# Kernel optimization log

Hardware: AMD Instinct MI355X
Metric: run time of the kernel (lower is better)

## Reference

```python
import jax, jax.numpy as jnp
import numpy as np

BS, C, H, W = 8, 128, 64, 64
CH = C // 2  # proj output channels


def setup_inputs() -> dict:
    key = jax.random.key(0)
    ks = jax.random.split(key, 8)
    s = 1.0 / np.sqrt(C)
    return {
        "tgt": jax.random.normal(ks[0], (BS, C, H, W), dtype=jnp.float32),
        "ref": jax.random.normal(ks[1], (BS, C, H, W), dtype=jnp.float32),
        "W_tgt": jax.random.normal(ks[2], (CH, C), dtype=jnp.float32) * s,
        "b_tgt": jax.random.normal(ks[3], (CH,), dtype=jnp.float32) * s,
        "W_ref": jax.random.normal(ks[4], (CH, C), dtype=jnp.float32) * s,
        "b_ref": jax.random.normal(ks[5], (CH,), dtype=jnp.float32) * s,
        "W_out": jax.random.normal(ks[6], (C, C), dtype=jnp.float32) * s,
        "b_out": jax.random.normal(ks[7], (C,), dtype=jnp.float32) * s,
    }


def reference(tgt, ref, W_tgt, b_tgt, W_ref, b_ref, W_out, b_out):
    bs, c, h, w = tgt.shape
    n = h * w
    # 1x1 conv == per-pixel matmul over channels; flatten spatial to tokens
    tgt_f = tgt.reshape(bs, c, n)              # [bs, c, n]
    ref_f = ref.reshape(bs, c, n)              # [bs, c, n]
    # att_tgt: [bs, n, c/2] ; att_ref: [bs, c/2, n] (ReLU after proj)
    att_tgt = jax.nn.relu(jnp.einsum('bcn,oc->bno', tgt_f, W_tgt) + b_tgt)
    att_ref = jax.nn.relu(jnp.einsum('bcn,oc->bon', ref_f, W_ref) + b_ref[None, :, None])
    pre_att = jnp.einsum('bnd,bdm->bnm', att_tgt, att_ref)   # [bs, n, n]
    att = jax.nn.softmax(pre_att, axis=-1)
    # fused tokens: [bs, n, c] = att @ ref_tokens
    fused = jnp.einsum('bnm,bcm->bnc', att, ref_f)
    fused = fused.transpose(0, 2, 1).reshape(bs, c, h, w)
    # output gate: 1x1 conv on tgt (no activation), elementwise mul
    att_out = jnp.einsum('bcn,oc->bon', tgt_f, W_out) + b_out[None, :, None]
    fused = fused * att_out.reshape(bs, c, h, w)
    return fused
```

## Files before the change

### kernel.cpp

```cpp
#include <hip/hip_runtime.h>

typedef __attribute__((ext_vector_type(8))) _Float16 f16x8;
typedef __attribute__((ext_vector_type(4))) float f32x4;

constexpr int kC  = 128;
constexpr int kCH = 64;
constexpr int kN  = 4096;
constexpr float kLog2e = 1.4426950408889634f;

__device__ __forceinline__ unsigned pkrtz(float a, float b) {
    union { __fp16 __attribute__((ext_vector_type(2))) v; unsigned u; } cv;
    cv.v = __builtin_amdgcn_cvt_pkrtz(a, b);
    return cv.u;
}

__device__ __forceinline__ float x2(float x) {
    return __builtin_amdgcn_exp2f(x);
}

__device__ __forceinline__ void g2l16(const unsigned short* g, unsigned short* l) {
    __builtin_amdgcn_global_load_lds(
        (const __attribute__((address_space(1))) unsigned int*)(g),
        (__attribute__((address_space(3))) unsigned int*)(l),
        16, 0, 0);
}

__global__ __launch_bounds__(256, 2) void proj_fused(
    const float* __restrict__ tgt, const float* __restrict__ ref,
    const float* __restrict__ Wt, const float* __restrict__ Wr,
    const float* __restrict__ Wo, const float* __restrict__ bt,
    const float* __restrict__ br, const float* __restrict__ bo,
    unsigned short* __restrict__ Qw, unsigned short* __restrict__ Kw,
    unsigned short* __restrict__ Vw, float* __restrict__ Gw)
{
    __shared__ __align__(16) unsigned short Xs[2][64 * 128];
    const int t = threadIdx.x;
    const int sl2 = blockIdx.y >> 3;
    const int b = blockIdx.y & 7;
    const int tok0 = blockIdx.x << 7;

    const int w = t >> 6, lane = t & 63;
    const int lg = (lane >> 4) & 3, lm = lane & 15;

    const float* X = sl2 ? ref : tgt;
    const float* Xb0 = X + ((size_t)b * kC) * kN + tok0;
    unsigned short* Vout = Vw + ((size_t)b * kC) * kN + tok0;

    const float* Wqk  = sl2 ? Wr : Wt;
    const float* bqk  = sl2 ? br : bt;
    const float scale = sl2 ? 1.0f : kLog2e;

    f16x8 wfq[4];
    float bq[4];
    {
        const int ocb = w * 16;
        #pragma unroll
        for (int ks = 0; ks < 4; ++ks) {
            const float* wp = Wqk + (size_t)(ocb + lm) * kC + ks * 32 + lg * 8;
            f32x4 f0 = *(const f32x4*)wp;
            f32x4 f1 = *(const f32x4*)(wp + 4);
            union { f16x8 h; uint4 u; } cv;
            cv.u = make_uint4(pkrtz(f0[0] * scale, f0[1] * scale),
                              pkrtz(f0[2] * scale, f0[3] * scale),
                              pkrtz(f1[0] * scale, f1[1] * scale),
                              pkrtz(f1[2] * scale, f1[3] * scale));
            wfq[ks] = cv.h;
        }
        #pragma unroll
        for (int r = 0; r < 4; ++r) bq[r] = bqk[ocb + lg * 4 + r] * scale;
    }

    f16x8 wfg[2][4];
    float bg[2][4];
    if (sl2 == 0) {
        const int ocb = w * 32;
        #pragma unroll
        for (int ot = 0; ot < 2; ++ot) {
            const int oc = ocb + ot * 16 + lm;
            #pragma unroll
            for (int ks = 0; ks < 4; ++ks) {
                const float* wp = Wo + (size_t)oc * kC + ks * 32 + lg * 8;
                f32x4 f0 = *(const f32x4*)wp;
                f32x4 f1 = *(const f32x4*)(wp + 4);
                union { f16x8 h; uint4 u; } cv;
                cv.u = make_uint4(pkrtz(f0[0], f0[1]), pkrtz(f0[2], f0[3]),
                                  pkrtz(f1[0], f1[1]), pkrtz(f1[2], f1[3]));
                wfg[ot][ks] = cv.h;
            }
            #pragma unroll
            for (int r = 0; r < 4; ++r) bg[ot][r] = bo[ocb + ot * 16 + lg * 4 + r];
        }
    }

    const int tk4 = (t & 15) * 4;
    const int c8  = (t >> 4) * 8;

    auto loadX = [&](int toff, f32x4* xv) {
        #pragma unroll
        for (int j = 0; j < 8; ++j)
            xv[j] = *(const f32x4*)(Xb0 + (size_t)(c8 + j) * kN + toff + tk4);
    };
    auto stageX = [&](const f32x4* xv, unsigned short* Xsb, int toff) {
        if (sl2 == 1) {
            #pragma unroll
            for (int j = 0; j < 8; ++j)
                *(uint2*)(Vout + (size_t)(c8 + j) * kN + toff + tk4) =
                    make_uint2(pkrtz(xv[j][0], xv[j][1]), pkrtz(xv[j][2], xv[j][3]));
        }
        #pragma unroll
        for (int s = 0; s < 4; ++s) {
            const int tok = tk4 + s;
            const int cc = (c8 >> 3) ^ (tok & 7);
            uint4 pk;
            pk.x = pkrtz(xv[0][s], xv[1][s]);
            pk.y = pkrtz(xv[2][s], xv[3][s]);
            pk.z = pkrtz(xv[4][s], xv[5][s]);
            pk.w = pkrtz(xv[6][s], xv[7][s]);
            *(uint4*)(Xsb + tok * 128 + cc * 8) = pk;
        }
    };
    auto compute = [&](const unsigned short* Xsb, int tokb) {
        unsigned short* outp = (sl2 ? Kw : Qw) + ((size_t)b * kN + tokb) * kCH;
        float* Gb = Gw + ((size_t)b * kC) * kN + tokb;
        const int ocq = w * 16;
        const int ocg = w * 32;
        #pragma unroll
        for (int ns = 0; ns < 4; ++ns) {
            const int tok = ns * 16 + lm;
            f16x8 xf[4];
            #pragma unroll
            for (int ks = 0; ks < 4; ++ks)
                xf[ks] = *(const f16x8*)(Xsb + tok * 128 +
                                         (((ks * 4 + lg) ^ (tok & 7)) << 3));
            {
                f32x4 acc = {bq[0], bq[1], bq[2], bq[3]};
                #pragma unroll
                for (int ks = 0; ks < 4; ++ks)
                    acc = __builtin_amdgcn_mfma_f32_16x16x32_f16(wfq[ks], xf[ks], acc, 0, 0, 0);
                uint2 pk;
                pk.x = pkrtz(fmaxf(acc[0], 0.f), fmaxf(acc[1], 0.f));
                pk.y = pkrtz(fmaxf(acc[2], 0.f), fmaxf(acc[3], 0.f));
                *(uint2*)(outp + (size_t)tok * kCH + ocq + lg * 4) = pk;
            }
            if (sl2 == 0) {
                #pragma unroll
                for (int ot = 0; ot < 2; ++ot) {
                    f32x4 acc = {bg[ot][0], bg[ot][1], bg[ot][2], bg[ot][3]};
                    #pragma unroll
                    for (int ks = 0; ks < 4; ++ks)
                        acc = __builtin_amdgcn_mfma_f32_16x16x32_f16(wfg[ot][ks], xf[ks], acc, 0, 0, 0);
                    #pragma unroll
                    for (int r = 0; r < 4; ++r)
                        Gb[(size_t)(ocg + ot * 16 + lg * 4 + r) * kN + tok] = acc[r];
                }
            }
        }
    };

    f32x4 xv[8], xw[8];
    loadX(0, xv);
    stageX(xv, Xs[0], 0);
    __syncthreads();
    loadX(64, xw);
    compute(Xs[0], tok0);
    stageX(xw, Xs[1], 64);
    __syncthreads();
    compute(Xs[1], tok0 + 64);
}

__global__ __launch_bounds__(256, 2) void flash7_kernel(
    const unsigned short* __restrict__ Qw,
    const unsigned short* __restrict__ Kw,
    const unsigned short* __restrict__ Vw,
    const float* __restrict__ Gw,
    float* __restrict__ out)
{
    __shared__ __align__(16) unsigned short Ks[2][64 * 64];
    __shared__ __align__(16) unsigned short Vs[2][128 * 64];
    __shared__ __align__(16) unsigned short Ps[64 * 64];

    const int t = threadIdx.x;
    const int b = blockIdx.x & 7;
    const int n0 = (blockIdx.x >> 3) << 6;
    const int w = t >> 6, lane = t & 63;
    const int lg = (lane >> 4) & 3, lm = lane & 15;
    const int row_q = w * 16 + lm;
    const int swz = lm & 7;

    const unsigned short* Qb = Qw + ((size_t)b * kN) * kCH;
    const unsigned short* Kb = Kw + ((size_t)b * kN) * kCH;
    const unsigned short* Vb = Vw + ((size_t)b * kC) * kN;

    f16x8 qf0 = *(const f16x8*)(Qb + (size_t)(n0 + row_q) * kCH + (lg << 3));
    f16x8 qf1 = *(const f16x8*)(Qb + (size_t)(n0 + row_q) * kCH + 32 + (lg << 3));

    const int srow = t >> 3, scol = t & 7;
    const int sco  = (scol ^ (srow & 7)) << 3;
    const int wv   = t >> 6;

    const int fswz0 = (lg ^ swz) << 3;
    const int fswz1 = ((4 | lg) ^ swz) << 3;
    int psw[4];
    #pragma unroll
    for (int mb = 0; mb < 4; ++mb)
        psw[mb] = row_q * 64 + (((2 * mb + (lg >> 1)) ^ swz) << 3) + ((lg & 1) << 2);

    union { f16x8 h; uint4 u; } onec;
    onec.u = make_uint4(0x3c003c00u, 0x3c003c00u, 0x3c003c00u, 0x3c003c00u);
    const f16x8 onev = onec.h;

    f32x4 O[8];
    #pragma unroll
    for (int cb = 0; cb < 8; ++cb) O[cb] = (f32x4){0.f, 0.f, 0.f, 0.f};
    f32x4 L = (f32x4){0.f, 0.f, 0.f, 0.f};
    float m_run = 0.0f;

    unsigned short* Ks0 = Ks[0]; unsigned short* Ks1 = Ks[1];
    unsigned short* Vs0 = Vs[0]; unsigned short* Vs1 = Vs[1];

    auto stage = [&](unsigned short* Kd, unsigned short* Vd, int m0) {
        g2l16(Kb + (size_t)(m0 + srow) * kCH + sco,      Kd + wv * 512);
        g2l16(Kb + (size_t)(m0 + 32 + srow) * kCH + sco, Kd + 2048 + wv * 512);
        #pragma unroll
        for (int j = 0; j < 4; ++j)
            g2l16(Vb + (size_t)(32 * j + srow) * kN + m0 + sco,
                  Vd + j * 2048 + wv * 512);
    };
    stage(Ks0, Vs0, 0);

    auto tile = [&](const unsigned short* Kc, const unsigned short* Vc,
                    unsigned short* Kn, unsigned short* Vn, int kt) {
        __syncthreads();
        if (kt + 1 < kN / 64) stage(Kn, Vn, (kt + 1) << 6);

        f32x4 s[4];
        __builtin_amdgcn_s_setprio(1);
        #pragma unroll
        for (int mb = 0; mb < 4; ++mb) {
            const unsigned short* kr = Kc + ((mb * 16 + lm) << 6);
            f16x8 kf0 = *(const f16x8*)(kr + fswz0);
            f16x8 kf1 = *(const f16x8*)(kr + fswz1);
            f32x4 acc = (f32x4){0.f, 0.f, 0.f, 0.f};
            acc = __builtin_amdgcn_mfma_f32_16x16x32_f16(kf0, qf0, acc, 0, 0, 0);
            acc = __builtin_amdgcn_mfma_f32_16x16x32_f16(kf1, qf1, acc, 0, 0, 0);
            s[mb] = acc;
        }
        __builtin_amdgcn_s_setprio(0);

        float mloc = 0.0f;
        #pragma unroll
        for (int mb = 0; mb < 4; ++mb)
            #pragma unroll
            for (int r = 0; r < 4; ++r) mloc = fmaxf(mloc, s[mb][r]);
        mloc = fmaxf(mloc, __shfl_xor(mloc, 16, 64));
        mloc = fmaxf(mloc, __shfl_xor(mloc, 32, 64));
        const bool upd = __any(mloc > m_run);
        const float mnew = upd ? fmaxf(m_run, mloc) : m_run;

        #pragma unroll
        for (int mb = 0; mb < 4; ++mb) {
            unsigned plo = pkrtz(x2(s[mb][0] - mnew), x2(s[mb][1] - mnew));
            unsigned phi = pkrtz(x2(s[mb][2] - mnew), x2(s[mb][3] - mnew));
            *(uint2*)(Ps + psw[mb]) = make_uint2(plo, phi);
        }

        if (upd) {
            float alpha = x2(m_run - mnew);
            float a0 = __shfl(alpha, (lg << 2) + 0, 64);
            float a1 = __shfl(alpha, (lg << 2) + 1, 64);
            float a2 = __shfl(alpha, (lg << 2) + 2, 64);
            float a3 = __shfl(alpha, (lg << 2) + 3, 64);
            #pragma unroll
            for (int cb = 0; cb < 8; ++cb) {
                O[cb][0] *= a0; O[cb][1] *= a1; O[cb][2] *= a2; O[cb][3] *= a3;
            }
            L[0] *= a0; L[1] *= a1; L[2] *= a2; L[3] *= a3;
            m_run = mnew;
        }

        f16x8 pf0 = *(const f16x8*)(Ps + row_q * 64 + fswz0);
        f16x8 pf1 = *(const f16x8*)(Ps + row_q * 64 + fswz1);
        __builtin_amdgcn_s_setprio(1);
        L = __builtin_amdgcn_mfma_f32_16x16x32_f16(pf0, onev, L, 0, 0, 0);
        L = __builtin_amdgcn_mfma_f32_16x16x32_f16(pf1, onev, L, 0, 0, 0);
        #pragma unroll
        for (int cb = 0; cb < 8; ++cb) {
            const unsigned short* vr = Vc + ((cb * 16 + lm) << 6);
            f16x8 vf0 = *(const f16x8*)(vr + fswz0);
            f16x8 vf1 = *(const f16x8*)(vr + fswz1);
            O[cb] = __builtin_amdgcn_mfma_f32_16x16x32_f16(pf0, vf0, O[cb], 0, 0, 0);
            O[cb] = __builtin_amdgcn_mfma_f32_16x16x32_f16(pf1, vf1, O[cb], 0, 0, 0);
        }
        __builtin_amdgcn_s_setprio(0);
    };

    for (int kt = 0; kt < kN / 64; kt += 2) {
        tile(Ks0, Vs0, Ks1, Vs1, kt);
        tile(Ks1, Vs1, Ks0, Vs0, kt + 1);
    }

    const float i0 = 1.0f / L[0], i1 = 1.0f / L[1];
    const float i2 = 1.0f / L[2], i3 = 1.0f / L[3];
    const float* Gb = Gw + ((size_t)b * kC) * kN;
    float* Ob = out + ((size_t)b * kC) * kN;
    #pragma unroll
    for (int cb = 0; cb < 8; ++cb) {
        int c = cb * 16 + lm;
        size_t base = (size_t)c * kN + n0 + w * 16 + (lg << 2);
        float4 g = *(const float4*)(Gb + base);
        float4 res;
        res.x = O[cb][0] * i0 * g.x;
        res.y = O[cb][1] * i1 * g.y;
        res.z = O[cb][2] * i2 * g.z;
        res.w = O[cb][3] * i3 * g.w;
        *(float4*)(Ob + base) = res;
    }
}

extern "C" void kernel_launch(void* const* d_in, const int* in_sizes, int n_in,
                              void* d_out, int out_size, void* d_ws, size_t ws_size,
                              hipStream_t stream) {
    const float* tgt   = (const float*)d_in[0];
    const float* ref   = (const float*)d_in[1];
    const float* W_tgt = (const float*)d_in[2];
    const float* b_tgt = (const float*)d_in[3];
    const float* W_ref = (const float*)d_in[4];
    const float* b_ref = (const float*)d_in[5];
    const float* W_out = (const float*)d_in[6];
    const float* b_out = (const float*)d_in[7];
    float* out = (float*)d_out;

    const size_t QK = (size_t)8 * kN * kCH;
    const size_t CV = (size_t)8 * kC * kN;
    unsigned short* Qw = (unsigned short*)d_ws;
    unsigned short* Kw = Qw + QK;
    unsigned short* Vw = Kw + QK;
    float*          Gw = (float*)(Vw + CV);

    proj_fused<<<dim3(32, 16), 256, 0, stream>>>(tgt, ref, W_tgt, W_ref, W_out,
                                                 b_tgt, b_ref, b_out, Qw, Kw, Vw, Gw);
    flash7_kernel<<<dim3(512), 256, 0, stream>>>(Qw, Kw, Vw, Gw, out);
}
```

Measured before the change: 183.4 us.

## Process two query sub-tiles per wave to double K/V reuse per block

Each wave now handles 32 query rows (two 16-row halves), so a block covers 128 queries instead of 64 and every K/V tile staged in shared memory feeds twice as many MFMAs. This halves global and LDS traffic for K and V per query. The cost is a doubled O accumulator set and more registers per thread, so launch bounds drop to one block per SM. The grid shrinks to 256 blocks, which may leave some of the 256 CUs underused or lower latency hiding.

```diff
diff --git a/kernel.cpp b/kernel.cpp
--- a/kernel.cpp
+++ b/kernel.cpp
@@ -168,7 +168,7 @@
     compute(Xs[1], tok0 + 64);
 }
 
-__global__ __launch_bounds__(256, 2) void flash7_kernel(
+__global__ __launch_bounds__(256, 1) void flash8_kernel(
     const unsigned short* __restrict__ Qw,
     const unsigned short* __restrict__ Kw,
     const unsigned short* __restrict__ Vw,
@@ -177,22 +177,27 @@
 {
     __shared__ __align__(16) unsigned short Ks[2][64 * 64];
     __shared__ __align__(16) unsigned short Vs[2][128 * 64];
-    __shared__ __align__(16) unsigned short Ps[64 * 64];
+    __shared__ __align__(16) unsigned short Ps[128 * 64];
 
     const int t = threadIdx.x;
     const int b = blockIdx.x & 7;
-    const int n0 = (blockIdx.x >> 3) << 6;
+    const int n0 = (blockIdx.x >> 3) << 7;
     const int w = t >> 6, lane = t & 63;
     const int lg = (lane >> 4) & 3, lm = lane & 15;
-    const int row_q = w * 16 + lm;
+    const int qw0 = w * 32;
     const int swz = lm & 7;
 
     const unsigned short* Qb = Qw + ((size_t)b * kN) * kCH;
     const unsigned short* Kb = Kw + ((size_t)b * kN) * kCH;
     const unsigned short* Vb = Vw + ((size_t)b * kC) * kN;
 
-    f16x8 qf0 = *(const f16x8*)(Qb + (size_t)(n0 + row_q) * kCH + (lg << 3));
-    f16x8 qf1 = *(const f16x8*)(Qb + (size_t)(n0 + row_q) * kCH + 32 + (lg << 3));
+    f16x8 qf[2][2];
+    #pragma unroll
+    for (int h = 0; h < 2; ++h) {
+        const unsigned short* qp = Qb + (size_t)(n0 + qw0 + h * 16 + lm) * kCH;
+        qf[h][0] = *(const f16x8*)(qp + (lg << 3));
+        qf[h][1] = *(const f16x8*)(qp + 32 + (lg << 3));
+    }
 
     const int srow = t >> 3, scol = t & 7;
     const int sco  = (scol ^ (srow & 7)) << 3;
@@ -200,20 +205,25 @@
 
     const int fswz0 = (lg ^ swz) << 3;
     const int fswz1 = ((4 | lg) ^ swz) << 3;
-    int psw[4];
+    int psw[2][4];
     #pragma unroll
-    for (int mb = 0; mb < 4; ++mb)
-        psw[mb] = row_q * 64 + (((2 * mb + (lg >> 1)) ^ swz) << 3) + ((lg & 1) << 2);
+    for (int h = 0; h < 2; ++h)
+        #pragma unroll
+        for (int mb = 0; mb < 4; ++mb)
+            psw[h][mb] = (qw0 + h * 16 + lm) * 64 +
+                         (((2 * mb + (lg >> 1)) ^ swz) << 3) + ((lg & 1) << 2);
 
     union { f16x8 h; uint4 u; } onec;
     onec.u = make_uint4(0x3c003c00u, 0x3c003c00u, 0x3c003c00u, 0x3c003c00u);
     const f16x8 onev = onec.h;
 
-    f32x4 O[8];
+    f32x4 O[2][8];
     #pragma unroll
-    for (int cb = 0; cb < 8; ++cb) O[cb] = (f32x4){0.f, 0.f, 0.f, 0.f};
-    f32x4 L = (f32x4){0.f, 0.f, 0.f, 0.f};
-    float m_run = 0.0f;
+    for (int h = 0; h < 2; ++h)
+        #pragma unroll
+        for (int cb = 0; cb < 8; ++cb) O[h][cb] = (f32x4){0.f, 0.f, 0.f, 0.f};
+    f32x4 L[2] = {(f32x4){0.f, 0.f, 0.f, 0.f}, (f32x4){0.f, 0.f, 0.f, 0.f}};
+    float m_run[2] = {0.0f, 0.0f};
 
     unsigned short* Ks0 = Ks[0]; unsigned short* Ks1 = Ks[1];
     unsigned short* Vs0 = Vs[0]; unsigned short* Vs1 = Vs[1];
@@ -233,63 +243,91 @@
         __syncthreads();
         if (kt + 1 < kN / 64) stage(Kn, Vn, (kt + 1) << 6);
 
-        f32x4 s[4];
+        f32x4 s[2][4];
         __builtin_amdgcn_s_setprio(1);
         #pragma unroll
         for (int mb = 0; mb < 4; ++mb) {
             const unsigned short* kr = Kc + ((mb * 16 + lm) << 6);
             f16x8 kf0 = *(const f16x8*)(kr + fswz0);
             f16x8 kf1 = *(const f16x8*)(kr + fswz1);
-            f32x4 acc = (f32x4){0.f, 0.f, 0.f, 0.f};
-            acc = __builtin_amdgcn_mfma_f32_16x16x32_f16(kf0, qf0, acc, 0, 0, 0);
-            acc = __builtin_amdgcn_mfma_f32_16x16x32_f16(kf1, qf1, acc, 0, 0, 0);
-            s[mb] = acc;
+            #pragma unroll
+            for (int h = 0; h < 2; ++h) {
+                f32x4 acc = (f32x4){0.f, 0.f, 0.f, 0.f};
+                acc = __builtin_amdgcn_mfma_f32_16x16x32_f16(kf0, qf[h][0], acc, 0, 0, 0);
+                acc = __builtin_amdgcn_mfma_f32_16x16x32_f16(kf1, qf[h][1], acc, 0, 0, 0);
+                s[h][mb] = acc;
+            }
         }
         __builtin_amdgcn_s_setprio(0);
 
-        float mloc = 0.0f;
-        #pragma unroll
-        for (int mb = 0; mb < 4; ++mb)
-            #pragma unroll
-            for (int r = 0; r < 4; ++r) mloc = fmaxf(mloc, s[mb][r]);
-        mloc = fmaxf(mloc, __shfl_xor(mloc, 16, 64));
-        mloc = fmaxf(mloc, __shfl_xor(mloc, 32, 64));
-        const bool upd = __any(mloc > m_run);
-        const float mnew = upd ? fmaxf(m_run, mloc) : m_run;
-
-        #pragma unroll
-        for (int mb = 0; mb < 4; ++mb) {
-            unsigned plo = pkrtz(x2(s[mb][0] - mnew), x2(s[mb][1] - mnew));
-            unsigned phi = pkrtz(x2(s[mb][2] - mnew), x2(s[mb][3] - mnew));
-            *(uint2*)(Ps + psw[mb]) = make_uint2(plo, phi);
-        }
+        float mloc[2];
+        #pragma unroll
+        for (int h = 0; h < 2; ++h) {
+            float m = 0.0f;
+            #pragma unroll
+            for (int mb = 0; mb < 4; ++mb)
+                #pragma unroll
+                for (int r = 0; r < 4; ++r) m = fmaxf(m, s[h][mb][r]);
+            m = fmaxf(m, __shfl_xor(m, 16, 64));
+            m = fmaxf(m, __shfl_xor(m, 32, 64));
+            mloc[h] = m;
+        }
+        const bool upd = __any((mloc[0] > m_run[0]) | (mloc[1] > m_run[1]));
+        float mnew[2];
+        #pragma unroll
+        for (int h = 0; h < 2; ++h)
+            mnew[h] = upd ? fmaxf(m_run[h], mloc[h]) : m_run[h];
+
+        #pragma unroll
+        for (int h = 0; h < 2; ++h)
+            #pragma unroll
+            for (int mb = 0; mb < 4; ++mb) {
+                unsigned plo = pkrtz(x2(s[h][mb][0] - mnew[h]), x2(s[h][mb][1] - mnew[h]));
+                unsigned phi = pkrtz(x2(s[h][mb][2] - mnew[h]), x2(s[h][mb][3] - mnew[h]));
+                *(uint2*)(Ps + psw[h][mb]) = make_uint2(plo, phi);
+            }
 
         if (upd) {
-            float alpha = x2(m_run - mnew);
-            float a0 = __shfl(alpha, (lg << 2) + 0, 64);
-            float a1 = __shfl(alpha, (lg << 2) + 1, 64);
-            float a2 = __shfl(alpha, (lg << 2) + 2, 64);
-            float a3 = __shfl(alpha, (lg << 2) + 3, 64);
-            #pragma unroll
-            for (int cb = 0; cb < 8; ++cb) {
-                O[cb][0] *= a0; O[cb][1] *= a1; O[cb][2] *= a2; O[cb][3] *= a3;
-            }
-            L[0] *= a0; L[1] *= a1; L[2] *= a2; L[3] *= a3;
-            m_run = mnew;
-        }
-
-        f16x8 pf0 = *(const f16x8*)(Ps + row_q * 64 + fswz0);
-        f16x8 pf1 = *(const f16x8*)(Ps + row_q * 64 + fswz1);
+            #pragma unroll
+            for (int h = 0; h < 2; ++h) {
+                float alpha = x2(m_run[h] - mnew[h]);
+                float a0 = __shfl(alpha, (lg << 2) + 0, 64);
+                float a1 = __shfl(alpha, (lg << 2) + 1, 64);
+                float a2 = __shfl(alpha, (lg << 2) + 2, 64);
+                float a3 = __shfl(alpha, (lg << 2) + 3, 64);
+                #pragma unroll
+                for (int cb = 0; cb < 8; ++cb) {
+                    O[h][cb][0] *= a0; O[h][cb][1] *= a1;
+                    O[h][cb][2] *= a2; O[h][cb][3] *= a3;
+                }
+                L[h][0] *= a0; L[h][1] *= a1; L[h][2] *= a2; L[h][3] *= a3;
+                m_run[h] = mnew[h];
+            }
+        }
+
+        f16x8 pf[2][2];
+        #pragma unroll
+        for (int h = 0; h < 2; ++h) {
+            const unsigned short* pr = Ps + (qw0 + h * 16 + lm) * 64;
+            pf[h][0] = *(const f16x8*)(pr + fswz0);
+            pf[h][1] = *(const f16x8*)(pr + fswz1);
+        }
         __builtin_amdgcn_s_setprio(1);
-        L = __builtin_amdgcn_mfma_f32_16x16x32_f16(pf0, onev, L, 0, 0, 0);
-        L = __builtin_amdgcn_mfma_f32_16x16x32_f16(pf1, onev, L, 0, 0, 0);
+        #pragma unroll
+        for (int h = 0; h < 2; ++h) {
+            L[h] = __builtin_amdgcn_mfma_f32_16x16x32_f16(pf[h][0], onev, L[h], 0, 0, 0);
+            L[h] = __builtin_amdgcn_mfma_f32_16x16x32_f16(pf[h][1], onev, L[h], 0, 0, 0);
+        }
         #pragma unroll
         for (int cb = 0; cb < 8; ++cb) {
             const unsigned short* vr = Vc + ((cb * 16 + lm) << 6);
             f16x8 vf0 = *(const f16x8*)(vr + fswz0);
             f16x8 vf1 = *(const f16x8*)(vr + fswz1);
-            O[cb] = __builtin_amdgcn_mfma_f32_16x16x32_f16(pf0, vf0, O[cb], 0, 0, 0);
-            O[cb] = __builtin_amdgcn_mfma_f32_16x16x32_f16(pf1, vf1, O[cb], 0, 0, 0);
+            #pragma unroll
+            for (int h = 0; h < 2; ++h) {
+                O[h][cb] = __builtin_amdgcn_mfma_f32_16x16x32_f16(pf[h][0], vf0, O[h][cb], 0, 0, 0);
+                O[h][cb] = __builtin_amdgcn_mfma_f32_16x16x32_f16(pf[h][1], vf1, O[h][cb], 0, 0, 0);
+            }
         }
         __builtin_amdgcn_s_setprio(0);
     };
@@ -299,21 +337,24 @@
         tile(Ks1, Vs1, Ks0, Vs0, kt + 1);
     }
 
-    const float i0 = 1.0f / L[0], i1 = 1.0f / L[1];
-    const float i2 = 1.0f / L[2], i3 = 1.0f / L[3];
     const float* Gb = Gw + ((size_t)b * kC) * kN;
     float* Ob = out + ((size_t)b * kC) * kN;
     #pragma unroll
-    for (int cb = 0; cb < 8; ++cb) {
-        int c = cb * 16 + lm;
-        size_t base = (size_t)c * kN + n0 + w * 16 + (lg << 2);
-        float4 g = *(const float4*)(Gb + base);
-        float4 res;
-        res.x = O[cb][0] * i0 * g.x;
-        res.y = O[cb][1] * i1 * g.y;
-        res.z = O[cb][2] * i2 * g.z;
-        res.w = O[cb][3] * i3 * g.w;
-        *(float4*)(Ob + base) = res;
+    for (int h = 0; h < 2; ++h) {
+        const float i0 = 1.0f / L[h][0], i1 = 1.0f / L[h][1];
+        const float i2 = 1.0f / L[h][2], i3 = 1.0f / L[h][3];
+        #pragma unroll
+        for (int cb = 0; cb < 8; ++cb) {
+            int c = cb * 16 + lm;
+            size_t base = (size_t)c * kN + n0 + qw0 + h * 16 + (lg << 2);
+            float4 g = *(const float4*)(Gb + base);
+            float4 res;
+            res.x = O[h][cb][0] * i0 * g.x;
+            res.y = O[h][cb][1] * i1 * g.y;
+            res.z = O[h][cb][2] * i2 * g.z;
+            res.w = O[h][cb][3] * i3 * g.w;
+            *(float4*)(Ob + base) = res;
+        }
     }
 }
 
@@ -339,5 +380,5 @@
 
     proj_fused<<<dim3(32, 16), 256, 0, stream>>>(tgt, ref, W_tgt, W_ref, W_out,
                                                  b_tgt, b_ref, b_out, Qw, Kw, Vw, Gw);
-    flash7_kernel<<<dim3(512), 256, 0, stream>>>(Qw, Kw, Vw, Gw, out);
-}
+    flash8_kernel<<<dim3(256), 256, 0, stream>>>(Qw, Kw, Vw, Gw, out);
+}
```

Result: slower. 209.8 us (+14.3%).

## Restructure flash attention with 32x32 MFMA, split-K waves and register P

Applied to the files above, without the earlier changes.

Rewrites the attention kernel to use 32x32x16 MFMA tiles. Each pair of waves handles the same 32 queries but different halves of every key tile, and their partial softmax states and outputs are merged through LDS at the end. P is now passed between lanes with shuffles instead of a round-trip through shared memory, and the row sum is accumulated with scalar adds instead of a ones-vector MFMA. Block-to-batch mapping also changes so consecutive blocks share a batch. The aim is fewer LDS writes and reads plus higher MFMA efficiency, at the cost of an extra merge phase, larger accumulators, and an uncoalesced strided epilogue store.

```diff
diff --git a/kernel.cpp b/kernel.cpp
--- a/kernel.cpp
+++ b/kernel.cpp
@@ -2,6 +2,7 @@
 
 typedef __attribute__((ext_vector_type(8))) _Float16 f16x8;
 typedef __attribute__((ext_vector_type(4))) float f32x4;
+typedef __attribute__((ext_vector_type(16))) float f32x16;
 
 constexpr int kC  = 128;
 constexpr int kCH = 64;
@@ -16,6 +17,11 @@
 
 __device__ __forceinline__ float x2(float x) {
     return __builtin_amdgcn_exp2f(x);
+}
+
+__device__ __forceinline__ float hadd2(unsigned u) {
+    union { unsigned v; _Float16 h[2]; } c; c.v = u;
+    return (float)c.h[0] + (float)c.h[1];
 }
 
 __device__ __forceinline__ void g2l16(const unsigned short* g, unsigned short* l) {
@@ -168,7 +174,7 @@
     compute(Xs[1], tok0 + 64);
 }
 
-__global__ __launch_bounds__(256, 2) void flash7_kernel(
+__global__ __launch_bounds__(256, 2) void flash10_kernel(
     const unsigned short* __restrict__ Qw,
     const unsigned short* __restrict__ Kw,
     const unsigned short* __restrict__ Vw,
@@ -177,43 +183,46 @@
 {
     __shared__ __align__(16) unsigned short Ks[2][64 * 64];
     __shared__ __align__(16) unsigned short Vs[2][128 * 64];
-    __shared__ __align__(16) unsigned short Ps[64 * 64];
+    __shared__ float2 mlb[4][32];
 
     const int t = threadIdx.x;
-    const int b = blockIdx.x & 7;
-    const int n0 = (blockIdx.x >> 3) << 6;
+    const int b  = blockIdx.x >> 6;
+    const int n0 = (blockIdx.x & 63) << 6;
     const int w = t >> 6, lane = t & 63;
-    const int lg = (lane >> 4) & 3, lm = lane & 15;
-    const int row_q = w * 16 + lm;
-    const int swz = lm & 7;
-
-    const unsigned short* Qb = Qw + ((size_t)b * kN) * kCH;
+    const int qg = w >> 1, kh = w & 1;
+    const int lq = lane & 31, hh = lane >> 5;
+    const int n0q = n0 + qg * 32 + lq;
+
+    const unsigned short* Qb = Qw + ((size_t)b * kN + n0q) * kCH;
     const unsigned short* Kb = Kw + ((size_t)b * kN) * kCH;
     const unsigned short* Vb = Vw + ((size_t)b * kC) * kN;
 
-    f16x8 qf0 = *(const f16x8*)(Qb + (size_t)(n0 + row_q) * kCH + (lg << 3));
-    f16x8 qf1 = *(const f16x8*)(Qb + (size_t)(n0 + row_q) * kCH + 32 + (lg << 3));
+    f16x8 qf[4];
+    #pragma unroll
+    for (int st = 0; st < 4; ++st)
+        qf[st] = *(const f16x8*)(Qb + st * 16 + hh * 8);
 
     const int srow = t >> 3, scol = t & 7;
     const int sco  = (scol ^ (srow & 7)) << 3;
     const int wv   = t >> 6;
 
-    const int fswz0 = (lg ^ swz) << 3;
-    const int fswz1 = ((4 | lg) ^ swz) << 3;
-    int psw[4];
-    #pragma unroll
-    for (int mb = 0; mb < 4; ++mb)
-        psw[mb] = row_q * 64 + (((2 * mb + (lg >> 1)) ^ swz) << 3) + ((lg & 1) << 2);
-
-    union { f16x8 h; uint4 u; } onec;
-    onec.u = make_uint4(0x3c003c00u, 0x3c003c00u, 0x3c003c00u, 0x3c003c00u);
-    const f16x8 onev = onec.h;
-
-    f32x4 O[8];
-    #pragma unroll
-    for (int cb = 0; cb < 8; ++cb) O[cb] = (f32x4){0.f, 0.f, 0.f, 0.f};
-    f32x4 L = (f32x4){0.f, 0.f, 0.f, 0.f};
-    float m_run = 0.0f;
+    int ka[4];
+    #pragma unroll
+    for (int st = 0; st < 4; ++st)
+        ka[st] = (kh * 32 + lq) * 64 + (((2 * st + hh) ^ (lq & 7)) << 3);
+    int va[4][2];
+    #pragma unroll
+    for (int cb = 0; cb < 4; ++cb)
+        #pragma unroll
+        for (int s = 0; s < 2; ++s)
+            va[cb][s] = (cb * 32 + lq) * 64 + (((kh * 4 + 2 * s + hh) ^ (lq & 7)) << 3);
+
+    f32x16 O[4];
+    #pragma unroll
+    for (int cb = 0; cb < 4; ++cb)
+        #pragma unroll
+        for (int r = 0; r < 16; ++r) O[cb][r] = 0.f;
+    float L = 0.f, m_run = 0.f;
 
     unsigned short* Ks0 = Ks[0]; unsigned short* Ks1 = Ks[1];
     unsigned short* Vs0 = Vs[0]; unsigned short* Vs1 = Vs[1];
@@ -233,63 +242,69 @@
         __syncthreads();
         if (kt + 1 < kN / 64) stage(Kn, Vn, (kt + 1) << 6);
 
-        f32x4 s[4];
+        f32x16 sa;
+        #pragma unroll
+        for (int r = 0; r < 16; ++r) sa[r] = 0.f;
         __builtin_amdgcn_s_setprio(1);
         #pragma unroll
-        for (int mb = 0; mb < 4; ++mb) {
-            const unsigned short* kr = Kc + ((mb * 16 + lm) << 6);
-            f16x8 kf0 = *(const f16x8*)(kr + fswz0);
-            f16x8 kf1 = *(const f16x8*)(kr + fswz1);
-            f32x4 acc = (f32x4){0.f, 0.f, 0.f, 0.f};
-            acc = __builtin_amdgcn_mfma_f32_16x16x32_f16(kf0, qf0, acc, 0, 0, 0);
-            acc = __builtin_amdgcn_mfma_f32_16x16x32_f16(kf1, qf1, acc, 0, 0, 0);
-            s[mb] = acc;
+        for (int st = 0; st < 4; ++st) {
+            f16x8 kf = *(const f16x8*)(Kc + ka[st]);
+            sa = __builtin_amdgcn_mfma_f32_32x32x16_f16(kf, qf[st], sa, 0, 0, 0);
         }
         __builtin_amdgcn_s_setprio(0);
 
-        float mloc = 0.0f;
-        #pragma unroll
-        for (int mb = 0; mb < 4; ++mb)
-            #pragma unroll
-            for (int r = 0; r < 4; ++r) mloc = fmaxf(mloc, s[mb][r]);
-        mloc = fmaxf(mloc, __shfl_xor(mloc, 16, 64));
-        mloc = fmaxf(mloc, __shfl_xor(mloc, 32, 64));
-        const bool upd = __any(mloc > m_run);
-        const float mnew = upd ? fmaxf(m_run, mloc) : m_run;
-
-        #pragma unroll
-        for (int mb = 0; mb < 4; ++mb) {
-            unsigned plo = pkrtz(x2(s[mb][0] - mnew), x2(s[mb][1] - mnew));
-            unsigned phi = pkrtz(x2(s[mb][2] - mnew), x2(s[mb][3] - mnew));
-            *(uint2*)(Ps + psw[mb]) = make_uint2(plo, phi);
-        }
+        float mh = sa[0];
+        #pragma unroll
+        for (int r = 1; r < 16; ++r) mh = fmaxf(mh, sa[r]);
+        float mq = fmaxf(mh, __shfl_xor(mh, 32));
+        const bool upd = __any(mq > m_run);
+        const float mnew = upd ? fmaxf(m_run, mq) : m_run;
+
+        #pragma unroll
+        for (int r = 0; r < 16; ++r) sa[r] = x2(sa[r] - mnew);
+        unsigned P[8];
+        #pragma unroll
+        for (int i = 0; i < 8; ++i) P[i] = pkrtz(sa[2 * i], sa[2 * i + 1]);
+
+        float ps = 0.f;
+        #pragma unroll
+        for (int i = 0; i < 8; ++i) ps += hadd2(P[i]);
+        ps += __shfl_xor(ps, 32);
 
         if (upd) {
-            float alpha = x2(m_run - mnew);
-            float a0 = __shfl(alpha, (lg << 2) + 0, 64);
-            float a1 = __shfl(alpha, (lg << 2) + 1, 64);
-            float a2 = __shfl(alpha, (lg << 2) + 2, 64);
-            float a3 = __shfl(alpha, (lg << 2) + 3, 64);
-            #pragma unroll
-            for (int cb = 0; cb < 8; ++cb) {
-                O[cb][0] *= a0; O[cb][1] *= a1; O[cb][2] *= a2; O[cb][3] *= a3;
-            }
-            L[0] *= a0; L[1] *= a1; L[2] *= a2; L[3] *= a3;
+            const float al = x2(m_run - mnew);
+            #pragma unroll
+            for (int cb = 0; cb < 4; ++cb) O[cb] *= al;
+            L = L * al + ps;
             m_run = mnew;
-        }
-
-        f16x8 pf0 = *(const f16x8*)(Ps + row_q * 64 + fswz0);
-        f16x8 pf1 = *(const f16x8*)(Ps + row_q * 64 + fswz1);
+        } else {
+            L += ps;
+        }
+
+        f16x8 pf[2];
+        #pragma unroll
+        for (int s = 0; s < 2; ++s) {
+            unsigned xa = __shfl_xor(P[4 * s + 0], 32);
+            unsigned xb = __shfl_xor(P[4 * s + 1], 32);
+            unsigned xc = __shfl_xor(P[4 * s + 2], 32);
+            unsigned xd = __shfl_xor(P[4 * s + 3], 32);
+            uint4 fu;
+            fu.x = hh ? xc : P[4 * s + 0];
+            fu.y = hh ? xd : P[4 * s + 1];
+            fu.z = hh ? P[4 * s + 2] : xa;
+            fu.w = hh ? P[4 * s + 3] : xb;
+            union { uint4 u; f16x8 h; } cv; cv.u = fu;
+            pf[s] = cv.h;
+        }
+
         __builtin_amdgcn_s_setprio(1);
-        L = __builtin_amdgcn_mfma_f32_16x16x32_f16(pf0, onev, L, 0, 0, 0);
-        L = __builtin_amdgcn_mfma_f32_16x16x32_f16(pf1, onev, L, 0, 0, 0);
-        #pragma unroll
-        for (int cb = 0; cb < 8; ++cb) {
-            const unsigned short* vr = Vc + ((cb * 16 + lm) << 6);
-            f16x8 vf0 = *(const f16x8*)(vr + fswz0);
-            f16x8 vf1 = *(const f16x8*)(vr + fswz1);
-            O[cb] = __builtin_amdgcn_mfma_f32_16x16x32_f16(pf0, vf0, O[cb], 0, 0, 0);
-            O[cb] = __builtin_amdgcn_mfma_f32_16x16x32_f16(pf1, vf1, O[cb], 0, 0, 0);
+        #pragma unroll
+        for (int cb = 0; cb < 4; ++cb) {
+            #pragma unroll
+            for (int s = 0; s < 2; ++s) {
+                f16x8 vf = *(const f16x8*)(Vc + va[cb][s]);
+                O[cb] = __builtin_amdgcn_mfma_f32_32x32x16_f16(vf, pf[s], O[cb], 0, 0, 0);
+            }
         }
         __builtin_amdgcn_s_setprio(0);
     };
@@ -299,21 +314,50 @@
         tile(Ks1, Vs1, Ks0, Vs0, kt + 1);
     }
 
-    const float i0 = 1.0f / L[0], i1 = 1.0f / L[1];
-    const float i2 = 1.0f / L[2], i3 = 1.0f / L[3];
-    const float* Gb = Gw + ((size_t)b * kC) * kN;
-    float* Ob = out + ((size_t)b * kC) * kN;
-    #pragma unroll
-    for (int cb = 0; cb < 8; ++cb) {
-        int c = cb * 16 + lm;
-        size_t base = (size_t)c * kN + n0 + w * 16 + (lg << 2);
-        float4 g = *(const float4*)(Gb + base);
-        float4 res;
-        res.x = O[cb][0] * i0 * g.x;
-        res.y = O[cb][1] * i1 * g.y;
-        res.z = O[cb][2] * i2 * g.z;
-        res.w = O[cb][3] * i3 * g.w;
-        *(float4*)(Ob + base) = res;
+    __syncthreads();
+    mlb[w][lq] = make_float2(m_run, L);
+    __syncthreads();
+    const float2 pml = mlb[w ^ 1][lq];
+    const float mt = fmaxf(m_run, pml.x);
+    const float a  = x2(m_run - mt);
+    const float Lt = L * a + pml.y * x2(pml.x - mt);
+
+    float* Obuf = (float*)Vs;
+    const int obase = qg * 4096 + lane * 64;
+    #pragma unroll
+    for (int cb = 0; cb < 4; ++cb) O[cb] *= a;
+
+    if (kh) {
+        #pragma unroll
+        for (int c = 0; c < 16; ++c) {
+            const int cb = c >> 2, q4 = c & 3;
+            *(float4*)(Obuf + obase + (((c + lane) & 15) << 2)) =
+                make_float4(O[cb][q4 * 4 + 0], O[cb][q4 * 4 + 1],
+                            O[cb][q4 * 4 + 2], O[cb][q4 * 4 + 3]);
+        }
+    }
+    __syncthreads();
+    if (!kh) {
+        #pragma unroll
+        for (int c = 0; c < 16; ++c) {
+            const int cb = c >> 2, q4 = c & 3;
+            float4 p = *(const float4*)(Obuf + obase + (((c + lane) & 15) << 2));
+            O[cb][q4 * 4 + 0] += p.x;
+            O[cb][q4 * 4 + 1] += p.y;
+            O[cb][q4 * 4 + 2] += p.z;
+            O[cb][q4 * 4 + 3] += p.w;
+        }
+        const float inv = 1.0f / Lt;
+        const float* Gb = Gw + ((size_t)b * kC + 4 * hh) * kN + n0 + qg * 32 + lq;
+        float*       Ob = out + ((size_t)b * kC + 4 * hh) * kN + n0 + qg * 32 + lq;
+        #pragma unroll
+        for (int cb = 0; cb < 4; ++cb) {
+            #pragma unroll
+            for (int r = 0; r < 16; ++r) {
+                const int coff = cb * 32 + (r & 3) + 8 * (r >> 2);
+                Ob[(size_t)coff * kN] = O[cb][r] * inv * Gb[(size_t)coff * kN];
+            }
+        }
     }
 }
 
@@ -339,5 +383,5 @@
 
     proj_fused<<<dim3(32, 16), 256, 0, stream>>>(tgt, ref, W_tgt, W_ref, W_out,
                                                  b_tgt, b_ref, b_out, Qw, Kw, Vw, Gw);
-    flash7_kernel<<<dim3(512), 256, 0, stream>>>(Qw, Kw, Vw, Gw, out);
-}
+    flash10_kernel<<<dim3(512), 256, 0, stream>>>(Qw, Kw, Vw, Gw, out);
+}
```

After: 186.5 us. No clear change (+1.7%).
